# Kernel optimization log

Hardware: AMD Instinct MI355X
Metric: run time of the kernel (lower is better)

Reference implementation:

```python
import jax, jax.numpy as jnp
import numpy as np

VQ_NUM = 3
EMB_NUM = 1024
COMMITMENT_WEIGHT = 1.0
# cumprod of [1, emb_num, emb_num] -> per-stage index bases
CUMPROD = [1, EMB_NUM, EMB_NUM * EMB_NUM]


def setup_inputs() -> dict:
    key = jax.random.key(0)
    k0, k1, k2, k3 = jax.random.split(key, 4)
    z = jax.random.normal(k0, (8, 4096, 512), dtype=jnp.float32)
    # linear_in: nn.Linear(in_ch=512, emb_ch=256, bias=False) -> weight [emb_ch, in_ch]
    W_in = jax.random.normal(k1, (VQ_NUM, 256, 512), dtype=jnp.float32) * 0.02
    # linear_out: nn.Linear(emb_ch=256, in_ch=512, bias=False) -> weight [in_ch, emb_ch]
    W_out = jax.random.normal(k2, (VQ_NUM, 512, 256), dtype=jnp.float32) * 0.02
    # one codebook per stage (share_residual_codebooks=False)
    codebooks = jax.random.normal(k3, (VQ_NUM, EMB_NUM, 256), dtype=jnp.float32) * 0.02
    return {"z": z, "W_in": W_in, "W_out": W_out, "codebooks": codebooks}


def reference(z, W_in, W_out, codebooks):
    sg = jax.lax.stop_gradient
    z_q = jnp.zeros_like(z)
    r = z
    loss = jnp.float32(0.0)
    index_sum = jnp.zeros(z.shape[:2], dtype=jnp.int64 if jax.config.jax_enable_x64 else jnp.int32)
    for i in range(VQ_NUM):
        # linear_in
        zi = jnp.einsum('bnc,ec->bne', r, W_in[i])  # [B,N,emb_ch]
        v = codebooks[i]  # [S, emb_ch]
        # squared L2 distance: ||z||^2 + ||v||^2 - 2 z.v
        dist = (jnp.sum(zi * zi, axis=-1, keepdims=True)
                + jnp.sum(v * v, axis=-1)
                - 2.0 * jnp.einsum('bne,se->bns', zi, v))  # [B,N,S]
        idx = jnp.argmin(dist, axis=-1)  # [B,N] int
        zq = v[idx]  # codebook lookup, [B,N,emb_ch]
        loss = loss + (COMMITMENT_WEIGHT * jnp.mean((sg(zq) - zi) ** 2)
                       + jnp.mean((zq - sg(zi)) ** 2))
        # straight-through estimator
        zq_ste = zi + sg(zq - zi)
        # linear_out
        r_q = jnp.einsum('bne,ce->bnc', zq_ste, W_out[i])  # [B,N,in_ch]
        index_sum = index_sum + idx.astype(index_sum.dtype) * CUMPROD[i]
        z_q = z_q + r_q
        r = z - sg(z_q)
    loss = loss / VQ_NUM + jnp.mean((z_q - z) ** 2)
    return z_q, index_sum, loss
```

## Files before the change

### kernel.cpp

```cpp
#include <hip/hip_runtime.h>

#define MTOK 32768
#define CIN  512
#define EMB  256
#define NCODE 1024
#define VQ   3
#define DELTA 2e-3f

typedef short s16x8 __attribute__((ext_vector_type(8)));
typedef float f32x4 __attribute__((ext_vector_type(4)));
typedef unsigned short u16;

static __device__ __forceinline__ u16 f2bf(float x) {
    unsigned int u = __float_as_uint(x);
    u += 0x7FFF + ((u >> 16) & 1);
    return (u16)(u >> 16);
}
static __device__ __forceinline__ float bf2f(u16 h) {
    return __uint_as_float(((unsigned int)h) << 16);
}

__global__ void init_k(double* loss_acc, int* cnt) {
    loss_acc[0] = 0.0;
    loss_acc[1] = 0.0;
    #pragma unroll
    for (int i = 0; i < 8; ++i) cnt[i] = 0;
}

__global__ __launch_bounds__(64) void prep_cb_k(const float* __restrict__ cbs,
                                                double* __restrict__ vnorm64,
                                                float* __restrict__ vnorm32,
                                                u16* __restrict__ cbh,
                                                u16* __restrict__ cbl) {
    int s = blockIdx.x;
    const float* row = cbs + (size_t)s * EMB;
    double acc = 0.0;
    for (int k = threadIdx.x; k < EMB; k += 64) {
        float v = row[k];
        double vd = (double)v; acc += vd * vd;
        u16 h = f2bf(v);
        u16 l = f2bf(v - bf2f(h));
        cbh[(size_t)s * EMB + k] = h;
        cbl[(size_t)s * EMB + k] = l;
    }
    #pragma unroll
    for (int off = 32; off > 0; off >>= 1) acc += __shfl_down(acc, off, 64);
    if (threadIdx.x == 0) { vnorm64[s] = acc; vnorm32[s] = (float)acc; }
}

__global__ __launch_bounds__(256) void prep_w_k(const float* __restrict__ W_in,
                                                u16* __restrict__ wh,
                                                u16* __restrict__ wl) {
    int i = blockIdx.x * 256 + threadIdx.x;
    float v = W_in[i];
    u16 h = f2bf(v);
    wh[i] = h;
    wl[i] = f2bf(v - bf2f(h));
}

__global__ __launch_bounds__(256) void prep_wt_k(const float* __restrict__ W_in,
                                                 float* __restrict__ WinT) {
    int i = blockIdx.x * 256 + threadIdx.x;
    int s = i / (EMB * CIN);
    int rem = i - s * (EMB * CIN);
    int e = rem / CIN;
    int k = rem - e * CIN;
    WinT[(size_t)s * CIN * EMB + (size_t)k * EMB + e] = W_in[i];
}

__global__ __launch_bounds__(256) void prep_T_k(const float* __restrict__ cbs,
                                                const float* __restrict__ Wout,
                                                float* __restrict__ T) {
    const int stage = blockIdx.z;
    const float* A = cbs  + (size_t)stage * NCODE * EMB;
    const float* B = Wout + (size_t)stage * CIN * EMB;
    float* C = T + (size_t)stage * NCODE * CIN;
    __shared__ float As[64][33];
    __shared__ float Bs[64][33];
    const int tid = threadIdx.x;
    const int ty = tid >> 4, tx = tid & 15;
    const int m0 = blockIdx.x * 64;
    const int n0 = blockIdx.y * 64;
    const int lrow = tid >> 5, lcol = tid & 31;
    double acc[4][4];
    #pragma unroll
    for (int i = 0; i < 4; ++i)
        #pragma unroll
        for (int j = 0; j < 4; ++j) acc[i][j] = 0.0;

    for (int k0 = 0; k0 < EMB; k0 += 32) {
        __syncthreads();
        #pragma unroll
        for (int t = 0; t < 8; ++t) {
            int r = lrow + 8 * t;
            As[r][lcol] = A[(size_t)(m0 + r) * EMB + k0 + lcol];
            Bs[r][lcol] = B[(size_t)(n0 + r) * EMB + k0 + lcol];
        }
        __syncthreads();
        #pragma unroll
        for (int k = 0; k < 32; ++k) {
            double a[4], b[4];
            #pragma unroll
            for (int i = 0; i < 4; ++i) a[i] = (double)As[ty * 4 + i][k];
            #pragma unroll
            for (int j = 0; j < 4; ++j) b[j] = (double)Bs[tx * 4 + j][k];
            #pragma unroll
            for (int i = 0; i < 4; ++i)
                #pragma unroll
                for (int j = 0; j < 4; ++j) acc[i][j] += a[i] * b[j];
        }
    }
    #pragma unroll
    for (int i = 0; i < 4; ++i) {
        float4 v = make_float4((float)acc[i][0], (float)acc[i][1],
                               (float)acc[i][2], (float)acc[i][3]);
        *reinterpret_cast<float4*>(&C[(size_t)(m0 + ty * 4 + i) * CIN + n0 + tx * 4]) = v;
    }
}

__global__ __launch_bounds__(256, 2) void zi_mfma_k(const float* __restrict__ z,
                                                    const float* __restrict__ zq,
                                                    const u16* __restrict__ wh,
                                                    const u16* __restrict__ wl,
                                                    float* __restrict__ zi,
                                                    double* __restrict__ loss_acc,
                                                    int stage0) {
    __shared__ __align__(16) u16 swh[2][16][520];
    __shared__ __align__(16) u16 swl[2][16][520];
    const int tid = threadIdx.x;
    const int w = tid >> 6;
    const int l = tid & 63;
    const int col = l & 15;
    const int g = l >> 4;
    const int mw = blockIdx.x * 64 + w * 16;
    const int sr = tid >> 4, sq = tid & 15;

    s16x8 ah[16], al[16];
    {
        const float* zr = z  + (size_t)(mw + col) * CIN + g * 8;
        const float* qr = zq + (size_t)(mw + col) * CIN + g * 8;
        #pragma unroll
        for (int kc = 0; kc < 16; ++kc) {
            float4 f0 = *reinterpret_cast<const float4*>(zr + kc * 32);
            float4 f1 = *reinterpret_cast<const float4*>(zr + kc * 32 + 4);
            float f[8] = {f0.x, f0.y, f0.z, f0.w, f1.x, f1.y, f1.z, f1.w};
            if (!stage0) {
                float4 q0 = *reinterpret_cast<const float4*>(qr + kc * 32);
                float4 q1 = *reinterpret_cast<const float4*>(qr + kc * 32 + 4);
                f[0] -= q0.x; f[1] -= q0.y; f[2] -= q0.z; f[3] -= q0.w;
                f[4] -= q1.x; f[5] -= q1.y; f[6] -= q1.z; f[7] -= q1.w;
            }
            #pragma unroll
            for (int j = 0; j < 8; ++j) {
                u16 h = f2bf(f[j]);
                u16 lo = f2bf(f[j] - bf2f(h));
                ah[kc][j] = (short)h; al[kc][j] = (short)lo;
            }
        }
    }

    const u16* gh = wh + (size_t)sr * CIN + sq * 8;
    const u16* gl = wl + (size_t)sr * CIN + sq * 8;
    uint4 h0, h1, h2, h3, l0, l1, l2, l3;
#define ZLOAD(NT) do { const u16* th = gh + (size_t)(NT) * (16 * CIN);                \
    const u16* tl = gl + (size_t)(NT) * (16 * CIN);                                   \
    h0 = *(const uint4*)(th);        h1 = *(const uint4*)(th + 128);                  \
    h2 = *(const uint4*)(th + 256);  h3 = *(const uint4*)(th + 384);                  \
    l0 = *(const uint4*)(tl);        l1 = *(const uint4*)(tl + 128);                  \
    l2 = *(const uint4*)(tl + 256);  l3 = *(const uint4*)(tl + 384); } while (0)
#define ZWRITE(P) do {                                                                \
    *(uint4*)&swh[P][sr][sq * 8]       = h0;  *(uint4*)&swh[P][sr][sq * 8 + 128] = h1;\
    *(uint4*)&swh[P][sr][sq * 8 + 256] = h2;  *(uint4*)&swh[P][sr][sq * 8 + 384] = h3;\
    *(uint4*)&swl[P][sr][sq * 8]       = l0;  *(uint4*)&swl[P][sr][sq * 8 + 128] = l1;\
    *(uint4*)&swl[P][sr][sq * 8 + 256] = l2;  *(uint4*)&swl[P][sr][sq * 8 + 384] = l3;\
    } while (0)
    ZLOAD(0); ZWRITE(0); ZLOAD(1);

    double zn = 0.0;
    for (int nt = 0; nt < 16; ++nt) {
        __syncthreads();
        const int p = nt & 1;
        if (nt + 1 < 16) ZWRITE((nt + 1) & 1);
        if (nt + 2 < 16) ZLOAD(nt + 2);
        f32x4 a0 = {0.f, 0.f, 0.f, 0.f};
        f32x4 a1 = {0.f, 0.f, 0.f, 0.f};
        f32x4 a2 = {0.f, 0.f, 0.f, 0.f};
        #pragma unroll
        for (int kc = 0; kc < 16; ++kc) {
            s16x8 Bh = *(const s16x8*)&swh[p][col][g * 8 + kc * 32];
            s16x8 Bl = *(const s16x8*)&swl[p][col][g * 8 + kc * 32];
            a0 = __builtin_amdgcn_mfma_f32_16x16x32_bf16(ah[kc], Bh, a0, 0, 0, 0);
            a1 = __builtin_amdgcn_mfma_f32_16x16x32_bf16(al[kc], Bh, a1, 0, 0, 0);
            a2 = __builtin_amdgcn_mfma_f32_16x16x32_bf16(ah[kc], Bl, a2, 0, 0, 0);
        }
        #pragma unroll
        for (int r = 0; r < 4; ++r) {
            float v = a0[r] + a1[r] + a2[r];
            zi[(size_t)(mw + g * 4 + r) * EMB + nt * 16 + col] = v;
            zn += (double)v * (double)v;
        }
    }
#undef ZLOAD
#undef ZWRITE
    #pragma unroll
    for (int off = 32; off > 0; off >>= 1) zn += __shfl_down(zn, off, 64);
    if (l == 0) atomicAdd(loss_acc, zn);
}

__global__ __launch_bounds__(256, 1) void pref_k(const float* __restrict__ zi,
                                                 const u16* __restrict__ cbh,
                                                 const u16* __restrict__ cbl,
                                                 const float* __restrict__ vnorm32,
                                                 int* __restrict__ idx,
                                                 int* __restrict__ idx_sum,
                                                 float* __restrict__ mind,
                                                 int* __restrict__ flagged,
                                                 int* __restrict__ cnt,
                                                 int* __restrict__ fullList,
                                                 int* __restrict__ cntF,
                                                 int* __restrict__ cand2,
                                                 double* __restrict__ loss_acc,
                                                 int stage0, int cumprod) {
    __shared__ __align__(16) u16 sbh[2][16][264];
    __shared__ __align__(16) u16 sbl[2][16][264];
    __shared__ double loss_s[16];
    const int tid = threadIdx.x;
    const int w = tid >> 6;
    const int l = tid & 63;
    const int col = l & 15;
    const int g = l >> 4;
    const int mw = blockIdx.x * 128 + w * 32;
    const int sr = tid >> 4, sq = tid & 15;

    s16x8 ah0[8], al0[8], ah1[8], al1[8];
    {
        const float* zr0 = zi + (size_t)(mw + col) * EMB + g * 8;
        const float* zr1 = zi + (size_t)(mw + 16 + col) * EMB + g * 8;
        #pragma unroll
        for (int kc = 0; kc < 8; ++kc) {
            float4 f0 = *reinterpret_cast<const float4*>(zr0 + kc * 32);
            float4 f1 = *reinterpret_cast<const float4*>(zr0 + kc * 32 + 4);
            float f[8] = {f0.x, f0.y, f0.z, f0.w, f1.x, f1.y, f1.z, f1.w};
            #pragma unroll
            for (int j = 0; j < 8; ++j) {
                u16 h = f2bf(f[j]);
                u16 lo = f2bf(f[j] - bf2f(h));
                ah0[kc][j] = (short)h;
                al0[kc][j] = (short)lo;
            }
            float4 e0 = *reinterpret_cast<const float4*>(zr1 + kc * 32);
            float4 e1 = *reinterpret_cast<const float4*>(zr1 + kc * 32 + 4);
            float e[8] = {e0.x, e0.y, e0.z, e0.w, e1.x, e1.y, e1.z, e1.w};
            #pragma unroll
            for (int j = 0; j < 8; ++j) {
                u16 h = f2bf(e[j]);
                u16 lo = f2bf(e[j] - bf2f(h));
                ah1[kc][j] = (short)h;
                al1[kc][j] = (short)lo;
            }
        }
    }

    float b1a[4], b2a[4], b3a[4], b1b[4], b2b[4], b3b[4];
    int   i1a[4], i2a[4], i1b[4], i2b[4];
    #pragma unroll
    for (int r = 0; r < 4; ++r) {
        b1a[r] = b2a[r] = b3a[r] = 1e30f; i1a[r] = i2a[r] = 0;
        b1b[r] = b2b[r] = b3b[r] = 1e30f; i1b[r] = i2b[r] = 0;
    }

    const u16* gh = cbh + (size_t)sr * EMB + sq * 8;
    const u16* gl = cbl + (size_t)sr * EMB + sq * 8;
    uint4 h0, h1, l0, l1;
#define PLOAD(CT) do { const u16* th = gh + (size_t)(CT) * (16 * EMB);                \
    const u16* tl = gl + (size_t)(CT) * (16 * EMB);                                   \
    h0 = *(const uint4*)(th);  h1 = *(const uint4*)(th + 128);                        \
    l0 = *(const uint4*)(tl);  l1 = *(const uint4*)(tl + 128); } while (0)
#define PWRITE(P) do {                                                                \
    *(uint4*)&sbh[P][sr][sq * 8] = h0;  *(uint4*)&sbh[P][sr][sq * 8 + 128] = h1;      \
    *(uint4*)&sbl[P][sr][sq * 8] = l0;  *(uint4*)&sbl[P][sr][sq * 8 + 128] = l1;      \
    } while (0)
    PLOAD(0); PWRITE(0); PLOAD(1);

    for (int ct = 0; ct < 64; ++ct) {
        __syncthreads();
        const int p = ct & 1;
        if (ct + 1 < 64) PWRITE((ct + 1) & 1);
        if (ct + 2 < 64) PLOAD(ct + 2);
        const float vn = vnorm32[ct * 16 + col];
        f32x4 a00 = {0.f, 0.f, 0.f, 0.f}, a01 = {0.f, 0.f, 0.f, 0.f}, a02 = {0.f, 0.f, 0.f, 0.f};
        f32x4 a10 = {0.f, 0.f, 0.f, 0.f}, a11 = {0.f, 0.f, 0.f, 0.f}, a12 = {0.f, 0.f, 0.f, 0.f};
        #pragma unroll
        for (int kc = 0; kc < 8; ++kc) {
            s16x8 Bh = *(const s16x8*)&sbh[p][col][g * 8 + kc * 32];
            s16x8 Bl = *(const s16x8*)&sbl[p][col][g * 8 + kc * 32];
            a00 = __builtin_amdgcn_mfma_f32_16x16x32_bf16(ah0[kc], Bh, a00, 0, 0, 0);
            a10 = __builtin_amdgcn_mfma_f32_16x16x32_bf16(ah1[kc], Bh, a10, 0, 0, 0);
            a01 = __builtin_amdgcn_mfma_f32_16x16x32_bf16(al0[kc], Bh, a01, 0, 0, 0);
            a11 = __builtin_amdgcn_mfma_f32_16x16x32_bf16(al1[kc], Bh, a11, 0, 0, 0);
            a02 = __builtin_amdgcn_mfma_f32_16x16x32_bf16(ah0[kc], Bl, a02, 0, 0, 0);
            a12 = __builtin_amdgcn_mfma_f32_16x16x32_bf16(ah1[kc], Bl, a12, 0, 0, 0);
        }
        #pragma unroll
        for (int r = 0; r < 4; ++r) {
            int c = ct * 16 + col;
            float sa = vn - 2.f * (a00[r] + a01[r] + a02[r]);
            if (sa < b1a[r]) { b3a[r] = b2a[r]; b2a[r] = b1a[r]; i2a[r] = i1a[r]; b1a[r] = sa; i1a[r] = c; }
            else if (sa < b2a[r]) { b3a[r] = b2a[r]; b2a[r] = sa; i2a[r] = c; }
            else b3a[r] = fminf(b3a[r], sa);
            float sb = vn - 2.f * (a10[r] + a11[r] + a12[r]);
            if (sb < b1b[r]) { b3b[r] = b2b[r]; b2b[r] = b1b[r]; i2b[r] = i1b[r]; b1b[r] = sb; i1b[r] = c; }
            else if (sb < b2b[r]) { b3b[r] = b2b[r]; b2b[r] = sb; i2b[r] = c; }
            else b3b[r] = fminf(b3b[r], sb);
        }
    }
#undef PLOAD
#undef PWRITE

#define MERGE16(B1, B2, B3, I1, I2) do {                                              \
    _Pragma("unroll")                                                                 \
    for (int off = 1; off < 16; off <<= 1) {                                          \
        _Pragma("unroll")                                                             \
        for (int r = 0; r < 4; ++r) {                                                 \
            float c1 = __shfl_xor(B1[r], off, 64);                                    \
            int   j1 = __shfl_xor(I1[r], off, 64);                                    \
            float c2 = __shfl_xor(B2[r], off, 64);                                    \
            int   j2 = __shfl_xor(I2[r], off, 64);                                    \
            float c3 = __shfl_xor(B3[r], off, 64);                                    \
            float nb1, nb2, nb3; int ni1, ni2;                                        \
            if (c1 < B1[r] || (c1 == B1[r] && j1 < I1[r])) {                          \
                nb1 = c1; ni1 = j1;                                                   \
                if (B1[r] < c2 || (B1[r] == c2 && I1[r] < j2)) {                      \
                    nb2 = B1[r]; ni2 = I1[r]; nb3 = fminf(B2[r], c2);                 \
                } else {                                                              \
                    nb2 = c2; ni2 = j2; nb3 = fminf(B1[r], c3);                       \
                }                                                                     \
            } else {                                                                  \
                nb1 = B1[r]; ni1 = I1[r];                                             \
                if (c1 < B2[r] || (c1 == B2[r] && j1 < I2[r])) {                      \
                    nb2 = c1; ni2 = j1; nb3 = fminf(B2[r], c2);                       \
                } else {                                                              \
                    nb2 = B2[r]; ni2 = I2[r]; nb3 = fminf(c1, B3[r]);                 \
                }                                                                     \
            }                                                                         \
            B1[r] = nb1; B2[r] = nb2; B3[r] = nb3; I1[r] = ni1; I2[r] = ni2;          \
        }                                                                             \
    }                                                                                 \
} while (0)
    MERGE16(b1a, b2a, b3a, i1a, i2a);
    MERGE16(b1b, b2b, b3b, i1b, i2b);
#undef MERGE16

    if (col == 0) {
        double lsum = 0.0;
        #pragma unroll
        for (int r = 0; r < 4; ++r) {
            int m = mw + g * 4 + r;
            idx[m] = i1a[r];
            if (stage0) idx_sum[m] = i1a[r];
            else        idx_sum[m] += i1a[r] * cumprod;
            mind[m] = b1a[r];
            lsum += (double)b1a[r];
            if (b2a[r] - b1a[r] < DELTA) {
                if (b3a[r] - b1a[r] < DELTA) {
                    int slot = atomicAdd(cntF, 1);
                    fullList[slot] = m;
                } else {
                    int slot = atomicAdd(cnt, 1);
                    flagged[slot] = m;
                    cand2[m] = i2a[r];
                }
            }
            int m2 = mw + 16 + g * 4 + r;
            idx[m2] = i1b[r];
            if (stage0) idx_sum[m2] = i1b[r];
            else        idx_sum[m2] += i1b[r] * cumprod;
            mind[m2] = b1b[r];
            lsum += (double)b1b[r];
            if (b2b[r] - b1b[r] < DELTA) {
                if (b3b[r] - b1b[r] < DELTA) {
                    int slot = atomicAdd(cntF, 1);
                    fullList[slot] = m2;
                } else {
                    int slot = atomicAdd(cnt, 1);
                    flagged[slot] = m2;
                    cand2[m2] = i2b[r];
                }
            }
        }
        loss_s[w * 4 + g] = lsum;
    }
    __syncthreads();
    if (tid == 0) {
        double s = 0.0;
        #pragma unroll
        for (int q = 0; q < 16; ++q) s += loss_s[q];
        atomicAdd(loss_acc, s);
    }
}

__global__ __launch_bounds__(256) void rescan_pair_k(const float* __restrict__ z,
                                                     const float* __restrict__ zqv,
                                                     const float* __restrict__ WinT,
                                                     const float* __restrict__ cb,
                                                     const double* __restrict__ vnorm64,
                                                     const int* __restrict__ flagged,
                                                     const int* __restrict__ cnt,
                                                     const int* __restrict__ cand2,
                                                     int* __restrict__ idx,
                                                     int* __restrict__ idx_sum,
                                                     float* __restrict__ mind,
                                                     double* __restrict__ loss_acc,
                                                     int cumprod, int stage0) {
    __shared__ double r64[8][CIN];
    __shared__ int mArr[8], cAArr[8], cBArr[8];
    double* zi_l = &r64[0][0];
    const int tid = threadIdx.x;
    const int w = tid >> 6, l = tid & 63;
    const int n = *cnt;

    for (int jb = blockIdx.x; jb * 8 < n; jb += gridDim.x) {
        const int nt = min(8, n - jb * 8);
        __syncthreads();
        if (tid < nt) {
            int m = flagged[jb * 8 + tid];
            mArr[tid] = m;
            cAArr[tid] = idx[m]; cBArr[tid] = cand2[m];
        }
        __syncthreads();
        for (int t = 0; t < nt; ++t) {
            const int m = mArr[t];
            #pragma unroll
            for (int h = 0; h < 2; ++h) {
                int k = tid + h * 256;
                float rv = z[(size_t)m * CIN + k];
                if (!stage0) rv -= zqv[(size_t)m * CIN + k];
                r64[t][k] = (double)rv;
            }
        }
        __syncthreads();
        double acc[8] = {0, 0, 0, 0, 0, 0, 0, 0};
        #pragma unroll 4
        for (int k = 0; k < CIN; ++k) {
            double wv = (double)WinT[(size_t)k * EMB + tid];
            #pragma unroll
            for (int t = 0; t < 8; ++t) acc[t] += r64[t][k] * wv;
        }
        __syncthreads();
        #pragma unroll
        for (int t = 0; t < 8; ++t) zi_l[t * 256 + tid] = acc[t];
        __syncthreads();

        for (int t = w; t < nt; t += 4) {
            const int cA = cAArr[t], cB = cBArr[t], m = mArr[t];
            const double* zt = zi_l + t * 256;
            float4 vA = *(const float4*)(cb + (size_t)cA * EMB + 4 * l);
            float4 vB = *(const float4*)(cb + (size_t)cB * EMB + 4 * l);
            double z0 = zt[4 * l], z1 = zt[4 * l + 1];
            double z2 = zt[4 * l + 2], z3 = zt[4 * l + 3];
            double sA = z0 * (double)vA.x + z1 * (double)vA.y
                      + z2 * (double)vA.z + z3 * (double)vA.w;
            double sB = z0 * (double)vB.x + z1 * (double)vB.y
                      + z2 * (double)vB.z + z3 * (double)vB.w;
            #pragma unroll
            for (int off = 1; off < 64; off <<= 1) {
                sA += __shfl_xor(sA, off, 64);
                sB += __shfl_xor(sB, off, 64);
            }
            if (l == 0) {
                double dA = vnorm64[cA] - 2.0 * sA;
                double dB = vnorm64[cB] - 2.0 * sB;
                int bi; double best;
                if (dB < dA || (dB == dA && cB < cA)) { bi = cB; best = dB; }
                else                                   { bi = cA; best = dA; }
                int oldI = idx[m];
                if (bi != oldI) { idx[m] = bi; idx_sum[m] += (bi - oldI) * cumprod; }
                atomicAdd(loss_acc, best - (double)mind[m]);
                mind[m] = (float)best;
            }
        }
    }
}

__global__ __launch_bounds__(256) void fullscan_k(const float* __restrict__ z,
                                                  const float* __restrict__ zqv,
                                                  const float* __restrict__ WinT,
                                                  const float* __restrict__ cb,
                                                  const double* __restrict__ vnorm64,
                                                  const int* __restrict__ fullList,
                                                  const int* __restrict__ cntF,
                                                  int* __restrict__ idx,
                                                  int* __restrict__ idx_sum,
                                                  float* __restrict__ mind,
                                                  double* __restrict__ loss_acc,
                                                  int cumprod, int stage0) {
    __shared__ double r64[CIN];
    __shared__ double zi64[EMB];
    __shared__ double sred[256];
    __shared__ int ired[256];
    const int tid = threadIdx.x;
    const int n = *cntF;

    for (int j = blockIdx.x; j < n; j += gridDim.x) {
        const int m = fullList[j];
        __syncthreads();
        #pragma unroll
        for (int h = 0; h < 2; ++h) {
            int k = tid + h * 256;
            float rv = z[(size_t)m * CIN + k];
            if (!stage0) rv -= zqv[(size_t)m * CIN + k];
            r64[k] = (double)rv;
        }
        __syncthreads();
        {
            double acc = 0.0;
            #pragma unroll 8
            for (int k = 0; k < CIN; ++k)
                acc += r64[k] * (double)WinT[(size_t)k * EMB + tid];
            zi64[tid] = acc;
        }
        __syncthreads();
        double best = 1e300; int bi = 0;
        #pragma unroll
        for (int q = 0; q < 4; ++q) {
            const int c = q * 256 + tid;
            const float* row = cb + (size_t)c * EMB;
            double s0 = 0, s1 = 0, s2 = 0, s3 = 0;
            #pragma unroll 4
            for (int e = 0; e < EMB; e += 4) {
                float4 v = *(const float4*)(row + e);
                s0 += zi64[e]     * (double)v.x;
                s1 += zi64[e + 1] * (double)v.y;
                s2 += zi64[e + 2] * (double)v.z;
                s3 += zi64[e + 3] * (double)v.w;
            }
            double sc = vnorm64[c] - 2.0 * ((s0 + s1) + (s2 + s3));
            if (sc < best) { best = sc; bi = c; }
        }
        sred[tid] = best; ired[tid] = bi;
        __syncthreads();
        for (int off = 128; off > 0; off >>= 1) {
            if (tid < off) {
                double ob = sred[tid + off]; int oi = ired[tid + off];
                if (ob < sred[tid] || (ob == sred[tid] && oi < ired[tid])) {
                    sred[tid] = ob; ired[tid] = oi;
                }
            }
            __syncthreads();
        }
        if (tid == 0) {
            int oldI = idx[m], bi2 = ired[0];
            double best2 = sred[0];
            if (bi2 != oldI) { idx[m] = bi2; idx_sum[m] += (bi2 - oldI) * cumprod; }
            atomicAdd(loss_acc, best2 - (double)mind[m]);
            mind[m] = (float)best2;
        }
    }
}

__global__ __launch_bounds__(256) void gather_k(const float* __restrict__ T,
                                                const int* __restrict__ idx,
                                                const float* __restrict__ z,
                                                float* __restrict__ zq,
                                                int stage0, int last,
                                                double* __restrict__ loss_acc) {
    __shared__ double red[256];
    int m = blockIdx.x * 16 + (threadIdx.x >> 4);
    int q = threadIdx.x & 15;
    const float* src = T + (size_t)idx[m] * CIN;
    float* dst = zq + (size_t)m * CIN;
    double s = 0.0;
    #pragma unroll
    for (int it = 0; it < 8; ++it) {
        int off = it * 64 + q * 4;
        float4 t = *reinterpret_cast<const float4*>(src + off);
        if (!stage0) {
            float4 o = *reinterpret_cast<const float4*>(dst + off);
            t.x += o.x; t.y += o.y; t.z += o.z; t.w += o.w;
        }
        *reinterpret_cast<float4*>(dst + off) = t;
        if (last) {
            float4 zv = *reinterpret_cast<const float4*>(z + (size_t)m * CIN + off);
            double d0 = (double)zv.x - (double)t.x;
            double d1 = (double)zv.y - (double)t.y;
            double d2 = (double)zv.z - (double)t.z;
            double d3 = (double)zv.w - (double)t.w;
            s += d0 * d0 + d1 * d1 + d2 * d2 + d3 * d3;
        }
    }
    if (last) {
        red[threadIdx.x] = s;
        __syncthreads();
        for (int off = 128; off > 0; off >>= 1) {
            if (threadIdx.x < off) red[threadIdx.x] += red[threadIdx.x + off];
            __syncthreads();
        }
        if (threadIdx.x == 0) atomicAdd(loss_acc + 1, red[0]);
    }
}

__global__ void final_k(const int* __restrict__ idx_sum,
                        const double* __restrict__ loss_acc,
                        float* __restrict__ out) {
    int i = blockIdx.x * blockDim.x + threadIdx.x;
    if (i < MTOK) out[MTOK * CIN + i] = (float)idx_sum[i];
    if (i == 0) {
        double loss = 2.0 * loss_acc[0] / (3.0 * (double)MTOK * (double)EMB)
                    + loss_acc[1] / ((double)MTOK * (double)CIN);
        out[MTOK * CIN + MTOK] = (float)loss;
    }
}

extern "C" void kernel_launch(void* const* d_in, const int* in_sizes, int n_in,
                              void* d_out, int out_size, void* d_ws, size_t ws_size,
                              hipStream_t stream) {
    const float* z     = (const float*)d_in[0];
    const float* W_in  = (const float*)d_in[1];
    const float* W_out = (const float*)d_in[2];
    const float* cbs   = (const float*)d_in[3];
    float* out = (float*)d_out;
    char* ws = (char*)d_ws;

    double* vnorm64  = (double*)ws;
    double* loss_acc = (double*)(ws + 24576);
    int*    cnt      = (int*)(ws + 24592);
    float*  vnorm32  = (float*)(ws + 24624);
    u16*    cbh      = (u16*)(ws + 36912);
    u16*    cbl      = (u16*)(ws + 1609776);
    u16*    wh       = (u16*)(ws + 3182640);
    u16*    wl       = (u16*)(ws + 3969072);
    float*  WinT     = (float*)(ws + 4755504);
    float*  T        = (float*)(ws + 6328368);
    float*  zi       = (float*)(ws + 12619824);
    char*   p        = ws + 46174256;
    int*    idx      = (int*)p;
    int*    idx_sum  = (int*)(p + 131072);
    int*    flagged  = (int*)(p + 262144);
    float*  mind     = (float*)(p + 393216);
    int*    cand2    = (int*)(p + 524288);
    int*    fullList = (int*)(p + 655360);

    float* zq = out;

    init_k<<<dim3(1), dim3(1), 0, stream>>>(loss_acc, cnt);
    prep_cb_k<<<dim3(VQ * NCODE), dim3(64), 0, stream>>>(cbs, vnorm64, vnorm32, cbh, cbl);
    prep_w_k<<<dim3(VQ * EMB * CIN / 256), dim3(256), 0, stream>>>(W_in, wh, wl);
    prep_wt_k<<<dim3(VQ * EMB * CIN / 256), dim3(256), 0, stream>>>(W_in, WinT);
    prep_T_k<<<dim3(NCODE / 64, CIN / 64, VQ), dim3(256), 0, stream>>>(cbs, W_out, T);

    const int cumprod[VQ] = {1, 1024, 1024 * 1024};
    for (int i = 0; i < VQ; ++i) {
        const float* cb = cbs + (size_t)i * NCODE * EMB;
        zi_mfma_k<<<dim3(MTOK / 64), dim3(256), 0, stream>>>(
            z, zq, wh + (size_t)i * EMB * CIN, wl + (size_t)i * EMB * CIN,
            zi, loss_acc, i == 0 ? 1 : 0);
        pref_k<<<dim3(MTOK / 128), dim3(256), 0, stream>>>(
            zi, cbh + (size_t)i * NCODE * EMB, cbl + (size_t)i * NCODE * EMB,
            vnorm32 + i * NCODE, idx, idx_sum, mind, flagged, cnt + i,
            fullList, cnt + 3 + i, cand2, loss_acc, i == 0 ? 1 : 0, cumprod[i]);
        rescan_pair_k<<<dim3(512), dim3(256), 0, stream>>>(
            z, zq, WinT + (size_t)i * EMB * CIN, cb, vnorm64 + i * NCODE,
            flagged, cnt + i, cand2, idx, idx_sum, mind, loss_acc, cumprod[i],
            i == 0 ? 1 : 0);
        fullscan_k<<<dim3(256), dim3(256), 0, stream>>>(
            z, zq, WinT + (size_t)i * EMB * CIN, cb, vnorm64 + i * NCODE,
            fullList, cnt + 3 + i, idx, idx_sum, mind, loss_acc, cumprod[i],
            i == 0 ? 1 : 0);
        gather_k<<<dim3(MTOK / 16), dim3(256), 0, stream>>>(
            T + (size_t)i * NCODE * CIN, idx, z, zq, i == 0 ? 1 : 0,
            i == VQ - 1 ? 1 : 0, loss_acc);
    }
    final_k<<<dim3(MTOK / 256), dim3(256), 0, stream>>>(idx_sum, loss_acc, out);
}
```

Baseline: 1.028 ms.

## Split codebook scan across two blocks per token tile and merge top-3 results

The distance prefilter kernel now splits the 1024-code codebook into two halves along a second grid dimension, doubling the block count. Each half writes its per-token top-3 distances and top-2 indices to scratch buffers. A new merge kernel combines the two halves, then does the index, flag and loss bookkeeping the prefilter used to do. This targets low occupancy on the 256-block grid, and launch bounds are raised to allow two blocks per CU. The cost is an extra kernel launch and scratch-buffer traffic, and the A operands are now converted twice.

```diff
diff --git a/kernel.cpp b/kernel.cpp
--- a/kernel.cpp
+++ b/kernel.cpp
@@ -207,29 +207,25 @@
     if (l == 0) atomicAdd(loss_acc, zn);
 }
 
-__global__ __launch_bounds__(256, 1) void pref_k(const float* __restrict__ zi,
+__global__ __launch_bounds__(256, 2) void pref_k(const float* __restrict__ zi,
                                                  const u16* __restrict__ cbh,
                                                  const u16* __restrict__ cbl,
                                                  const float* __restrict__ vnorm32,
-                                                 int* __restrict__ idx,
-                                                 int* __restrict__ idx_sum,
-                                                 float* __restrict__ mind,
-                                                 int* __restrict__ flagged,
-                                                 int* __restrict__ cnt,
-                                                 int* __restrict__ fullList,
-                                                 int* __restrict__ cntF,
-                                                 int* __restrict__ cand2,
-                                                 double* __restrict__ loss_acc,
-                                                 int stage0, int cumprod) {
+                                                 float* __restrict__ pb1,
+                                                 float* __restrict__ pb2,
+                                                 float* __restrict__ pb3,
+                                                 int* __restrict__ pi1,
+                                                 int* __restrict__ pi2) {
     __shared__ __align__(16) u16 sbh[2][16][264];
     __shared__ __align__(16) u16 sbl[2][16][264];
-    __shared__ double loss_s[16];
     const int tid = threadIdx.x;
     const int w = tid >> 6;
     const int l = tid & 63;
     const int col = l & 15;
     const int g = l >> 4;
     const int mw = blockIdx.x * 128 + w * 32;
+    const int half = blockIdx.y;
+    const int ct0 = half * 32;
     const int sr = tid >> 4, sq = tid & 15;
 
     s16x8 ah0[8], al0[8], ah1[8], al1[8];
@@ -280,13 +276,13 @@
     *(uint4*)&sbh[P][sr][sq * 8] = h0;  *(uint4*)&sbh[P][sr][sq * 8 + 128] = h1;      \
     *(uint4*)&sbl[P][sr][sq * 8] = l0;  *(uint4*)&sbl[P][sr][sq * 8 + 128] = l1;      \
     } while (0)
-    PLOAD(0); PWRITE(0); PLOAD(1);
-
-    for (int ct = 0; ct < 64; ++ct) {
+    PLOAD(ct0); PWRITE(0); PLOAD(ct0 + 1);
+
+    for (int ct = ct0; ct < ct0 + 32; ++ct) {
         __syncthreads();
         const int p = ct & 1;
-        if (ct + 1 < 64) PWRITE((ct + 1) & 1);
-        if (ct + 2 < 64) PLOAD(ct + 2);
+        if (ct + 1 < ct0 + 32) PWRITE((ct + 1) & 1);
+        if (ct + 2 < ct0 + 32) PLOAD(ct + 2);
         const float vn = vnorm32[ct * 16 + col];
         f32x4 a00 = {0.f, 0.f, 0.f, 0.f}, a01 = {0.f, 0.f, 0.f, 0.f}, a02 = {0.f, 0.f, 0.f, 0.f};
         f32x4 a10 = {0.f, 0.f, 0.f, 0.f}, a11 = {0.f, 0.f, 0.f, 0.f}, a12 = {0.f, 0.f, 0.f, 0.f};
@@ -352,51 +348,73 @@
 #undef MERGE16
 
     if (col == 0) {
-        double lsum = 0.0;
+        const size_t base = (size_t)half * MTOK;
         #pragma unroll
         for (int r = 0; r < 4; ++r) {
-            int m = mw + g * 4 + r;
-            idx[m] = i1a[r];
-            if (stage0) idx_sum[m] = i1a[r];
-            else        idx_sum[m] += i1a[r] * cumprod;
-            mind[m] = b1a[r];
-            lsum += (double)b1a[r];
-            if (b2a[r] - b1a[r] < DELTA) {
-                if (b3a[r] - b1a[r] < DELTA) {
-                    int slot = atomicAdd(cntF, 1);
-                    fullList[slot] = m;
-                } else {
-                    int slot = atomicAdd(cnt, 1);
-                    flagged[slot] = m;
-                    cand2[m] = i2a[r];
-                }
-            }
-            int m2 = mw + 16 + g * 4 + r;
-            idx[m2] = i1b[r];
-            if (stage0) idx_sum[m2] = i1b[r];
-            else        idx_sum[m2] += i1b[r] * cumprod;
-            mind[m2] = b1b[r];
-            lsum += (double)b1b[r];
-            if (b2b[r] - b1b[r] < DELTA) {
-                if (b3b[r] - b1b[r] < DELTA) {
-                    int slot = atomicAdd(cntF, 1);
-                    fullList[slot] = m2;
-                } else {
-                    int slot = atomicAdd(cnt, 1);
-                    flagged[slot] = m2;
-                    cand2[m2] = i2b[r];
-                }
-            }
-        }
-        loss_s[w * 4 + g] = lsum;
-    }
+            size_t o = base + mw + g * 4 + r;
+            pb1[o] = b1a[r]; pb2[o] = b2a[r]; pb3[o] = b3a[r];
+            pi1[o] = i1a[r]; pi2[o] = i2a[r];
+            size_t o2 = base + mw + 16 + g * 4 + r;
+            pb1[o2] = b1b[r]; pb2[o2] = b2b[r]; pb3[o2] = b3b[r];
+            pi1[o2] = i1b[r]; pi2[o2] = i2b[r];
+        }
+    }
+}
+
+__global__ __launch_bounds__(256) void merge_k(const float* __restrict__ pb1,
+                                               const float* __restrict__ pb2,
+                                               const float* __restrict__ pb3,
+                                               const int* __restrict__ pi1,
+                                               const int* __restrict__ pi2,
+                                               int* __restrict__ idx,
+                                               int* __restrict__ idx_sum,
+                                               float* __restrict__ mind,
+                                               int* __restrict__ flagged,
+                                               int* __restrict__ cnt,
+                                               int* __restrict__ fullList,
+                                               int* __restrict__ cntF,
+                                               int* __restrict__ cand2,
+                                               double* __restrict__ loss_acc,
+                                               int stage0, int cumprod) {
+    __shared__ double red[256];
+    const int m = blockIdx.x * 256 + threadIdx.x;
+    float a1 = pb1[m], a2 = pb2[m], a3 = pb3[m];
+    int   ja1 = pi1[m], ja2 = pi2[m];
+    float e1 = pb1[MTOK + m], e2 = pb2[MTOK + m], e3 = pb3[MTOK + m];
+    int   je1 = pi1[MTOK + m], je2 = pi2[MTOK + m];
+
+    bool aF = (a1 < e1) || (a1 == e1 && ja1 < je1);
+    float m1 = aF ? a1 : e1;  int j1 = aF ? ja1 : je1;
+    float x  = aF ? a2 : a1;  int jx = aF ? ja2 : ja1;
+    float y  = aF ? e1 : e2;  int jy = aF ? je1 : je2;
+    bool aF2 = (x < y) || (x == y && jx < jy);
+    float m2 = aF2 ? x : y;   int j2 = aF2 ? jx : jy;
+    int ta = (aF ? 1 : 0) + (aF2 ? 1 : 0);
+    float an = (ta == 0) ? a1 : ((ta == 1) ? a2 : a3);
+    float en = (ta == 2) ? e1 : ((ta == 1) ? e2 : e3);
+    float m3 = fminf(an, en);
+
+    idx[m] = j1;
+    if (stage0) idx_sum[m] = j1;
+    else        idx_sum[m] += j1 * cumprod;
+    mind[m] = m1;
+    if (m2 - m1 < DELTA) {
+        if (m3 - m1 < DELTA) {
+            int slot = atomicAdd(cntF, 1);
+            fullList[slot] = m;
+        } else {
+            int slot = atomicAdd(cnt, 1);
+            flagged[slot] = m;
+            cand2[m] = j2;
+        }
+    }
+    red[threadIdx.x] = (double)m1;
     __syncthreads();
-    if (tid == 0) {
-        double s = 0.0;
-        #pragma unroll
-        for (int q = 0; q < 16; ++q) s += loss_s[q];
-        atomicAdd(loss_acc, s);
-    }
+    for (int off = 128; off > 0; off >>= 1) {
+        if (threadIdx.x < off) red[threadIdx.x] += red[threadIdx.x + off];
+        __syncthreads();
+    }
+    if (threadIdx.x == 0) atomicAdd(loss_acc, red[0]);
 }
 
 __global__ __launch_bounds__(256) void rescan_pair_k(const float* __restrict__ z,
@@ -639,6 +657,12 @@
     float*  mind     = (float*)(p + 393216);
     int*    cand2    = (int*)(p + 524288);
     int*    fullList = (int*)(p + 655360);
+    char*   q        = p + 786432;
+    float*  pb1      = (float*)q;
+    float*  pb2      = (float*)(q + 262144);
+    float*  pb3      = (float*)(q + 524288);
+    int*    pi1      = (int*)(q + 786432);
+    int*    pi2      = (int*)(q + 1048576);
 
     float* zq = out;
 
@@ -654,9 +678,11 @@
         zi_mfma_k<<<dim3(MTOK / 64), dim3(256), 0, stream>>>(
             z, zq, wh + (size_t)i * EMB * CIN, wl + (size_t)i * EMB * CIN,
             zi, loss_acc, i == 0 ? 1 : 0);
-        pref_k<<<dim3(MTOK / 128), dim3(256), 0, stream>>>(
+        pref_k<<<dim3(MTOK / 128, 2), dim3(256), 0, stream>>>(
             zi, cbh + (size_t)i * NCODE * EMB, cbl + (size_t)i * NCODE * EMB,
-            vnorm32 + i * NCODE, idx, idx_sum, mind, flagged, cnt + i,
+            vnorm32 + i * NCODE, pb1, pb2, pb3, pi1, pi2);
+        merge_k<<<dim3(MTOK / 256), dim3(256), 0, stream>>>(
+            pb1, pb2, pb3, pi1, pi2, idx, idx_sum, mind, flagged, cnt + i,
             fullList, cnt + 3 + i, cand2, loss_acc, i == 0 ? 1 : 0, cumprod[i]);
         rescan_pair_k<<<dim3(512), dim3(256), 0, stream>>>(
             z, zq, WinT + (size_t)i * EMB * CIN, cb, vnorm64 + i * NCODE,
```

After: 989.5 us. 1.04x faster.
